# Kernel tuning notes

Hardware: AMD Instinct MI355X
Metric: run time of the kernel (lower is better)

The kernel has to match this reference:

```python
import jax, jax.numpy as jnp
import numpy as np
import math

B, N, D, K = 8, 2048, 1024, 128
PI = math.pi


def setup_inputs() -> dict:
    key = jax.random.key(0)
    ks = jax.random.split(key, 4)
    x = jax.random.normal(ks[0], (B, N, D), dtype=jnp.float32)
    W_proj = jax.random.normal(ks[1], (D, 6 * K), dtype=jnp.float32) * (D ** -0.5)
    # structured bias init as in OscillatorProjection._init_weights
    b = np.zeros(6 * K, np.float32)
    groups = [K // 4, K // 2, K - K // 4 - K // 2]
    centers = [0.3, 0.65, 0.97]
    off = 3 * K
    for n_k, c in zip(groups, centers):
        b[off:off + n_k] = math.log(c / (1.0 - c))
        off += n_k
    b[4 * K:5 * K] = math.log(0.65 / 0.35)
    b[5 * K:] = -2.0
    b_proj = jnp.asarray(b)
    omega_base = jnp.exp(jnp.linspace(math.log(2.0 * PI / N), math.log(PI * (1.0 - 1.0 / K)), K)).astype(jnp.float32)
    W_phase = jax.random.normal(ks[2], (D, K), dtype=jnp.float32) * 0.001
    b_phase = jnp.zeros((K,), jnp.float32)
    W_res = jax.random.normal(ks[3], (4 * K - 2, D), dtype=jnp.float32) * 0.002
    lambda_pcg = jnp.float32(0.5)
    res_scale = jnp.float32(0.05)
    return dict(x=x, W_proj=W_proj, b_proj=b_proj, omega_base=omega_base,
                W_phase=W_phase, b_phase=b_phase, W_res=W_res,
                lambda_pcg=lambda_pcg, res_scale=res_scale)


def _resonance_scan(alpha, drive):
    # linear recurrence r_t = alpha_t * r_{t-1} + d_t, r_0 = 0, along axis=1
    def combine(e1, e2):
        a1, b1 = e1
        a2, b2 = e2
        return (a2 * a1, a2 * b1 + b2)
    _, r = jax.lax.associative_scan(combine, (alpha, drive), axis=1)
    return r


def reference(x, W_proj, b_proj, omega_base, W_phase, b_phase, W_res, lambda_pcg, res_scale):
    _, n, _ = x.shape
    out = x @ W_proj + b_proj  # [B, n, 6K]
    A_r, Om_r, Ph_r, Ga_r, Go_r, Be_r = jnp.split(out, 6, axis=-1)
    A = jnp.minimum(jax.nn.softplus(A_r), 3.0)
    omega = jnp.clip(jax.nn.sigmoid(Om_r) * PI + omega_base, 1e-4, PI - 1e-4)
    phi = jnp.tanh(Ph_r) * PI
    alpha = jax.nn.sigmoid(Ga_r)
    g_out = jax.nn.sigmoid(Go_r)
    beta = jax.nn.sigmoid(Be_r)
    positions = jnp.log1p(jnp.arange(n, dtype=jnp.float32)).reshape(1, n, 1)
    angle = omega * positions + phi
    cos_a = jnp.cos(angle)
    sin_a = jnp.sin(angle)
    drive = (1.0 - alpha) * A
    # fused real/imag scan sharing alpha (mirrors the fused Triton path)
    r = _resonance_scan(jnp.concatenate([alpha, alpha], axis=-1),
                        jnp.concatenate([drive * cos_a, drive * sin_a], axis=-1))
    r_r, r_i = r[..., :K], r[..., K:]
    readout = r_r * cos_a + r_i * sin_a
    r_r = r_r - beta * readout * cos_a
    r_i = r_i - beta * readout * sin_a
    # state norm: rescale only when |r| > 1
    modulus = jnp.sqrt(r_r ** 2 + r_i ** 2 + 1e-8)
    scale = jnp.maximum(modulus, 1.0)
    r_r = r_r / scale
    r_i = r_i / scale
    # rotate into the oscillator frame
    rho_re = r_r * cos_a + r_i * sin_a
    rho_im = -r_r * sin_a + r_i * cos_a
    rho_norm = jnp.sqrt(rho_re ** 2 + rho_im ** 2 + 1e-6)
    pq = x @ W_phase + b_phase
    align = (rho_re * jnp.cos(pq) + rho_im * jnp.sin(pq)) / rho_norm
    gate = jax.nn.sigmoid(lambda_pcg * align)
    rho_re = gate * rho_re
    rho_im = gate * rho_im
    # SCPM: adjacent-oscillator complex cross products -> 4K-2 features
    cross_re = rho_re[..., :-1] * rho_re[..., 1:] + rho_im[..., :-1] * rho_im[..., 1:]
    cross_im = rho_im[..., :-1] * rho_re[..., 1:] - rho_re[..., :-1] * rho_im[..., 1:]
    feats = jnp.concatenate([g_out * rho_re, g_out * rho_im, cross_re, cross_im], axis=-1)
    return x + res_scale * (feats @ W_res)
```

## Files before the change

### kernel.cpp

```cpp
#include <hip/hip_runtime.h>
#include <math.h>

#define PI_F 3.14159265358979323846f
#define SEG 128
#define SLEN 16
typedef unsigned short u16;
typedef __attribute__((ext_vector_type(8))) short bf16x8;
typedef __attribute__((ext_vector_type(4))) float f32x4;

__device__ __forceinline__ float sigmoidf_(float x){ return __fdividef(1.0f, 1.0f+__expf(-x)); }
__device__ __forceinline__ float softplusf_(float x){
    return fmaxf(x, 0.f) + __logf(1.f + __expf(-fabsf(x)));
}
__device__ __forceinline__ float tanhpi_(float x){
    float t = __expf(-2.f*fabsf(x));
    float th = __fdividef(1.f - t, 1.f + t);
    return copysignf(th, x)*PI_F;
}
__device__ __forceinline__ void fsincos(float a, float* s, float* c){
    float r = a * 0.15915494309189535f;
    r = r - floorf(r);
#if __has_builtin(__builtin_amdgcn_sinf)
    *s = __builtin_amdgcn_sinf(r);
    *c = __builtin_amdgcn_cosf(r);
#else
    float t = r * 6.283185307179586f;
    *s = __sinf(t); *c = __cosf(t);
#endif
}
__device__ __forceinline__ u16 f2bf(float f){
    unsigned u = __float_as_uint(f);
    return (u16)((u + 0x7FFFu + ((u>>16)&1u)) >> 16);
}
__device__ __forceinline__ float b2f(u16 v){
    return __uint_as_float(((unsigned)v)<<16);
}
__device__ __forceinline__ void gl_lds16(const u16* g, u16* l){
    __builtin_amdgcn_global_load_lds((const __attribute__((address_space(1))) void*)g,
                                     (__attribute__((address_space(3))) void*)l, 16, 0, 0);
}

__global__ __launch_bounds__(256) void k_cvt_x(const float* __restrict__ x, u16* __restrict__ xb){
    size_t i = ((size_t)blockIdx.x*256 + threadIdx.x)*8;
    float4 v0 = *(const float4*)&x[i];
    float4 v1 = *(const float4*)&x[i+4];
    ushort4 a = make_ushort4(f2bf(v0.x),f2bf(v0.y),f2bf(v0.z),f2bf(v0.w));
    ushort4 b = make_ushort4(f2bf(v1.x),f2bf(v1.y),f2bf(v1.z),f2bf(v1.w));
    *(ushort4*)&xb[i]   = a;
    *(ushort4*)&xb[i+4] = b;
}

__global__ __launch_bounds__(256) void k_tcvt(const float* __restrict__ W, u16* __restrict__ Wt,
                                              int K, int Ns, int KD){
    __shared__ float s[32][33];
    const int tx = threadIdx.x & 31, ty = threadIdx.x >> 5;
    const int k0 = blockIdx.y*32, n0 = blockIdx.x*32;
    #pragma unroll
    for (int i=0;i<4;i++){
        int k = k0 + ty + i*8;
        s[ty+i*8][tx] = (k < K) ? W[(size_t)k*Ns + n0 + tx] : 0.f;
    }
    __syncthreads();
    #pragma unroll
    for (int i=0;i<4;i++){
        int n = n0 + ty + i*8;
        Wt[(size_t)n*KD + k0 + tx] = f2bf(s[tx][ty+i*8]);
    }
}

__global__ __launch_bounds__(256) void k_mm1(
    const u16* __restrict__ A,
    const u16* __restrict__ Bt,
    const float* __restrict__ bp, const float* __restrict__ bph,
    u16* __restrict__ C)
{
    const int bid = blockIdx.x;
    const int swz = (bid & 7)*112 + (bid >> 3);
    const int by = swz / 7, bx = swz - by*7;

    __shared__ u16 As[128*32];
    __shared__ u16 Bs[128*32];
    const int tid = threadIdx.x;
    const int w = tid>>6, lane = tid&63;
    const int wm = w>>1, wn = w&1;
    const int r0 = by*128, c0 = bx*128;

    const u16* ga[2]; const u16* gb[2]; u16 *la[2], *lb[2];
    #pragma unroll
    for (int i=0;i<2;i++){
        ga[i] = A  + (size_t)(r0 + w*32 + i*16 + (lane>>2))*1024 + (lane&3)*8;
        gb[i] = Bt + (size_t)(c0 + w*32 + i*16 + (lane>>2))*1024 + (lane&3)*8;
        la[i] = As + w*1024 + i*512;
        lb[i] = Bs + w*1024 + i*512;
    }
    const int lr = lane&15, lk = lane>>4;
    const int ao = (wm*64 + lr)*32 + lk*8;
    const int bo = (wn*64 + lr)*32 + lk*8;

    f32x4 acc[4][4] = {};
    for (int k0=0; k0<1024; k0+=32){
        gl_lds16(ga[0]+k0, la[0]); gl_lds16(ga[1]+k0, la[1]);
        gl_lds16(gb[0]+k0, lb[0]); gl_lds16(gb[1]+k0, lb[1]);
        __syncthreads();
        bf16x8 af[4], bfr[4];
        #pragma unroll
        for (int m=0;m<4;m++) af[m]  = *(const bf16x8*)&As[ao + m*512];
        #pragma unroll
        for (int n=0;n<4;n++) bfr[n] = *(const bf16x8*)&Bs[bo + n*512];
        #pragma unroll
        for (int m=0;m<4;m++)
            #pragma unroll
            for (int n=0;n<4;n++)
                acc[m][n] = __builtin_amdgcn_mfma_f32_16x16x32_bf16(af[m], bfr[n], acc[m][n], 0,0,0);
        __syncthreads();
    }
    #pragma unroll
    for (int n=0;n<4;n++){
        int col = c0 + wn*64 + n*16 + lr;
        float bl = (col < 768) ? bp[col] : bph[col-768];
        #pragma unroll
        for (int m=0;m<4;m++){
            int row = r0 + wm*64 + m*16 + lk*4;
            #pragma unroll
            for (int r=0;r<4;r++)
                C[(size_t)(row+r)*896 + col] = f2bf(acc[m][n][r] + bl);
        }
    }
}

__global__ __launch_bounds__(256) void k_mm2(
    const u16* __restrict__ A,
    const u16* __restrict__ Bt,
    const float* __restrict__ X,
    const float* __restrict__ rs_p,
    float* __restrict__ O)
{
    const int bid = blockIdx.x;
    const int swz = (bid & 7)*128 + (bid >> 3);
    const int by = swz >> 3, bx = swz & 7;

    __shared__ u16 As[128*32];
    __shared__ u16 Bs[128*32];
    const int tid = threadIdx.x;
    const int w = tid>>6, lane = tid&63;
    const int wm = w>>1, wn = w&1;
    const int r0 = by*128, c0 = bx*128;

    const u16* ga[2]; const u16* gb[2]; u16 *la[2], *lb[2];
    #pragma unroll
    for (int i=0;i<2;i++){
        ga[i] = A  + (size_t)(r0 + w*32 + i*16 + (lane>>2))*512 + (lane&3)*8;
        gb[i] = Bt + (size_t)(c0 + w*32 + i*16 + (lane>>2))*512 + (lane&3)*8;
        la[i] = As + w*1024 + i*512;
        lb[i] = Bs + w*1024 + i*512;
    }
    const int lr = lane&15, lk = lane>>4;
    const int ao = (wm*64 + lr)*32 + lk*8;
    const int bo = (wn*64 + lr)*32 + lk*8;

    f32x4 acc[4][4] = {};
    for (int k0=0; k0<512; k0+=32){
        gl_lds16(ga[0]+k0, la[0]); gl_lds16(ga[1]+k0, la[1]);
        gl_lds16(gb[0]+k0, lb[0]); gl_lds16(gb[1]+k0, lb[1]);
        __syncthreads();
        bf16x8 af[4], bfr[4];
        #pragma unroll
        for (int m=0;m<4;m++) af[m]  = *(const bf16x8*)&As[ao + m*512];
        #pragma unroll
        for (int n=0;n<4;n++) bfr[n] = *(const bf16x8*)&Bs[bo + n*512];
        #pragma unroll
        for (int m=0;m<4;m++)
            #pragma unroll
            for (int n=0;n<4;n++)
                acc[m][n] = __builtin_amdgcn_mfma_f32_16x16x32_bf16(af[m], bfr[n], acc[m][n], 0,0,0);
        __syncthreads();
    }
    const float rs = rs_p[0];
    #pragma unroll
    for (int n=0;n<4;n++){
        int col = c0 + wn*64 + n*16 + lr;
        #pragma unroll
        for (int m=0;m<4;m++){
            int row = r0 + wm*64 + m*16 + lk*4;
            #pragma unroll
            for (int r=0;r<4;r++){
                size_t idx = (size_t)(row+r)*1024 + col;
                O[idx] = X[idx] + rs*acc[m][n][r];
            }
        }
    }
}

__global__ __launch_bounds__(128) void k_s1(
    const u16* __restrict__ C1,
    const float* __restrict__ omega_base,
    float* __restrict__ Ag, float* __restrict__ Br, float* __restrict__ Bi)
{
    const int k = threadIdx.x;
    const int seg = blockIdx.x, b = blockIdx.y;
    const float ob = omega_base[k];
    const int n0 = seg*SLEN;
    float aag = 1.f, br = 0.f, bi = 0.f;
    #pragma unroll 4
    for (int s=0; s<SLEN; s++){
        const int n = n0 + s;
        const u16* row = C1 + (size_t)(b*2048+n)*896;
        float Ar = b2f(row[k]);
        float Om = b2f(row[128+k]);
        float Ph = b2f(row[256+k]);
        float Ga = b2f(row[384+k]);
        float alpha = sigmoidf_(Ga);
        float A = fminf(softplusf_(Ar), 3.0f);
        float omega = fminf(fmaxf(sigmoidf_(Om)*PI_F + ob, 1e-4f), PI_F-1e-4f);
        float phi = tanhpi_(Ph);
        float pos = __logf(1.f + (float)n);
        float sa, ca; fsincos(fmaf(omega, pos, phi), &sa, &ca);
        float drive = (1.f-alpha)*A;
        aag *= alpha;
        br = fmaf(alpha, br, drive*ca);
        bi = fmaf(alpha, bi, drive*sa);
    }
    const size_t o = (size_t)(b*SEG + seg)*128 + k;
    Ag[o] = aag; Br[o] = br; Bi[o] = bi;
}

__global__ __launch_bounds__(256) void k_s2(
    const float* __restrict__ Ag, const float* __restrict__ Br, const float* __restrict__ Bi,
    float* __restrict__ Pr, float* __restrict__ Pi)
{
    const int gid = blockIdx.x*256 + threadIdx.x;
    const int b = gid >> 7, k = gid & 127;
    float pr = 0.f, pi = 0.f;
    #pragma unroll 8
    for (int seg=0; seg<SEG; seg++){
        const size_t o = (size_t)(b*SEG + seg)*128 + k;
        float a = Ag[o], r = Br[o], i = Bi[o];
        Pr[o] = pr; Pi[o] = pi;
        pr = fmaf(a, pr, r);
        pi = fmaf(a, pi, i);
    }
}

__global__ __launch_bounds__(128) void k_s3(
    const u16* __restrict__ C1,
    const float* __restrict__ omega_base,
    const float* __restrict__ lam_p,
    const float* __restrict__ Pr, const float* __restrict__ Pi,
    u16* __restrict__ F)
{
    const int k = threadIdx.x;
    const int seg = blockIdx.x, b = blockIdx.y;
    const float ob = omega_base[k];
    const float lam = lam_p[0];
    __shared__ float sre[2][129], sim[2][129];

    const size_t po = (size_t)(b*SEG + seg)*128 + k;
    float rr = Pr[po], ri = Pi[po];
    const int n0 = seg*SLEN;

    #pragma unroll 2
    for (int s=0; s<SLEN; s++){
        const int n = n0 + s;
        const u16* row = C1 + (size_t)(b*2048+n)*896;
        float Ar = b2f(row[k]);
        float Om = b2f(row[128+k]);
        float Ph = b2f(row[256+k]);
        float Ga = b2f(row[384+k]);
        float Go = b2f(row[512+k]);
        float Be = b2f(row[640+k]);
        float pq = b2f(row[768+k]);
        float alpha = sigmoidf_(Ga);
        float A = fminf(softplusf_(Ar), 3.0f);
        float omega = fminf(fmaxf(sigmoidf_(Om)*PI_F + ob, 1e-4f), PI_F-1e-4f);
        float phi = tanhpi_(Ph);
        float pos = __logf(1.f + (float)n);
        float sa, ca; fsincos(fmaf(omega, pos, phi), &sa, &ca);
        float drive = (1.f-alpha)*A;
        rr = fmaf(alpha, rr, drive*ca);
        ri = fmaf(alpha, ri, drive*sa);
        float readout = rr*ca + ri*sa;
        float beta = sigmoidf_(Be);
        float r2r = rr - beta*readout*ca;
        float r2i = ri - beta*readout*sa;
        float m2 = r2r*r2r + r2i*r2i + 1e-8f;
        float inv = fminf(rsqrtf(m2), 1.0f);
        r2r *= inv; r2i *= inv;
        float rho_re =  r2r*ca + r2i*sa;
        float rho_im = -r2r*sa + r2i*ca;
        float rho2 = rho_re*rho_re + rho_im*rho_im + 1e-6f;
        float spq, cpq; fsincos(pq, &spq, &cpq);
        float align = (rho_re*cpq + rho_im*spq)*rsqrtf(rho2);
        float gate = sigmoidf_(lam*align);
        rho_re *= gate; rho_im *= gate;
        float go = sigmoidf_(Go);

        const int buf = s & 1;
        sre[buf][k] = rho_re; sim[buf][k] = rho_im;
        __syncthreads();

        u16* frow = F + (size_t)(b*2048+n)*512;
        frow[k]       = f2bf(go*rho_re);
        frow[128 + k] = f2bf(go*rho_im);
        if (k < 127){
            float nre = sre[buf][k+1], nim = sim[buf][k+1];
            frow[256 + k] = f2bf(rho_re*nre + rho_im*nim);
            frow[383 + k] = f2bf(rho_im*nre - rho_re*nim);
        } else {
            frow[510] = 0; frow[511] = 0;
        }
    }
}

extern "C" void kernel_launch(void* const* d_in, const int* in_sizes, int n_in,
                              void* d_out, int out_size, void* d_ws, size_t ws_size,
                              hipStream_t stream)
{
    const float* x   = (const float*)d_in[0];
    const float* Wp  = (const float*)d_in[1];
    const float* bp  = (const float*)d_in[2];
    const float* ob  = (const float*)d_in[3];
    const float* Wph = (const float*)d_in[4];
    const float* bph = (const float*)d_in[5];
    const float* Wr  = (const float*)d_in[6];
    const float* lam = (const float*)d_in[7];
    const float* rs  = (const float*)d_in[8];
    float* out = (float*)d_out;

    char* ws = (char*)d_ws;
    u16*   C1  = (u16*)  (ws + 0);
    u16*   Xb  = (u16*)  (ws + 58720256);
    float* Ag  = (float*)(ws + 58720256);
    float* Brr = (float*)(ws + 58720256 +  524288);
    float* Bii = (float*)(ws + 58720256 + 1048576);
    float* Pr  = (float*)(ws + 58720256 + 1572864);
    float* Pi  = (float*)(ws + 58720256 + 2097152);
    u16*   F   = (u16*)  (ws + 58720256 + 2621440);
    u16*   Wt  = (u16*)  (ws + 92274688);
    u16*   Wrt = (u16*)  (ws + 94109696);

    dim3 blk(256);
    hipLaunchKernelGGL(k_cvt_x, dim3(8192),   blk, 0, stream, x, Xb);
    hipLaunchKernelGGL(k_tcvt,  dim3(24,32),  blk, 0, stream, Wp,  Wt,            1024, 768,  1024);
    hipLaunchKernelGGL(k_tcvt,  dim3(4,32),   blk, 0, stream, Wph, Wt + 768*1024, 1024, 128,  1024);
    hipLaunchKernelGGL(k_tcvt,  dim3(32,16),  blk, 0, stream, Wr,  Wrt,           510,  1024, 512);
    hipLaunchKernelGGL(k_mm1,   dim3(896),    blk, 0, stream, Xb, Wt, bp, bph, C1);
    hipLaunchKernelGGL(k_s1,    dim3(SEG,8),  dim3(128), 0, stream, C1, ob, Ag, Brr, Bii);
    hipLaunchKernelGGL(k_s2,    dim3(4),      blk, 0, stream, Ag, Brr, Bii, Pr, Pi);
    hipLaunchKernelGGL(k_s3,    dim3(SEG,8),  dim3(128), 0, stream, C1, ob, lam, Pr, Pi, F);
    hipLaunchKernelGGL(k_mm2,   dim3(1024),   blk, 0, stream, F, Wrt, x, rs, out);
}
```

Measured before the change: 152.7 us.

## Fuse three scan kernels into one cooperative kernel with grid syncs and LDS staging

Replaces the three-pass segmented scan (local reduce, carry propagation, apply) with a single cooperative kernel. Each block stages its 16×896 bf16 slice of C1 in shared memory once, so the second pass no longer rereads global memory. Two grid-wide syncs separate the phases, and only 8 blocks run the serial carry scan. The workspace buffers are moved so the bf16 copy of x stays alive, and the final GEMM epilogue now reads that bf16 x instead of fp32 x. That lowers residual precision and adds grid-sync overhead plus a co-residency requirement for 1024 blocks.

After: 318.4 us. 109% more time.

```diff
diff --git a/kernel.cpp b/kernel.cpp
--- a/kernel.cpp
+++ b/kernel.cpp
@@ -1,11 +1,15 @@
 #include <hip/hip_runtime.h>
+#include <hip/hip_cooperative_groups.h>
 #include <math.h>
+
+namespace cg = cooperative_groups;
 
 #define PI_F 3.14159265358979323846f
 #define SEG 128
 #define SLEN 16
 typedef unsigned short u16;
 typedef __attribute__((ext_vector_type(8))) short bf16x8;
+typedef __attribute__((ext_vector_type(8))) unsigned short u16x8;
 typedef __attribute__((ext_vector_type(4))) float f32x4;
 
 __device__ __forceinline__ float sigmoidf_(float x){ return __fdividef(1.0f, 1.0f+__expf(-x)); }
@@ -131,7 +135,7 @@
 __global__ __launch_bounds__(256) void k_mm2(
     const u16* __restrict__ A,
     const u16* __restrict__ Bt,
-    const float* __restrict__ X,
+    const u16* __restrict__ Xb,
     const float* __restrict__ rs_p,
     float* __restrict__ O)
 {
@@ -185,90 +189,92 @@
             #pragma unroll
             for (int r=0;r<4;r++){
                 size_t idx = (size_t)(row+r)*1024 + col;
-                O[idx] = X[idx] + rs*acc[m][n][r];
+                O[idx] = b2f(Xb[idx]) + rs*acc[m][n][r];
             }
         }
     }
 }
 
-__global__ __launch_bounds__(128) void k_s1(
-    const u16* __restrict__ C1,
-    const float* __restrict__ omega_base,
-    float* __restrict__ Ag, float* __restrict__ Br, float* __restrict__ Bi)
-{
-    const int k = threadIdx.x;
-    const int seg = blockIdx.x, b = blockIdx.y;
-    const float ob = omega_base[k];
-    const int n0 = seg*SLEN;
-    float aag = 1.f, br = 0.f, bi = 0.f;
-    #pragma unroll 4
-    for (int s=0; s<SLEN; s++){
-        const int n = n0 + s;
-        const u16* row = C1 + (size_t)(b*2048+n)*896;
-        float Ar = b2f(row[k]);
-        float Om = b2f(row[128+k]);
-        float Ph = b2f(row[256+k]);
-        float Ga = b2f(row[384+k]);
-        float alpha = sigmoidf_(Ga);
-        float A = fminf(softplusf_(Ar), 3.0f);
-        float omega = fminf(fmaxf(sigmoidf_(Om)*PI_F + ob, 1e-4f), PI_F-1e-4f);
-        float phi = tanhpi_(Ph);
-        float pos = __logf(1.f + (float)n);
-        float sa, ca; fsincos(fmaf(omega, pos, phi), &sa, &ca);
-        float drive = (1.f-alpha)*A;
-        aag *= alpha;
-        br = fmaf(alpha, br, drive*ca);
-        bi = fmaf(alpha, bi, drive*sa);
-    }
-    const size_t o = (size_t)(b*SEG + seg)*128 + k;
-    Ag[o] = aag; Br[o] = br; Bi[o] = bi;
-}
-
-__global__ __launch_bounds__(256) void k_s2(
-    const float* __restrict__ Ag, const float* __restrict__ Br, const float* __restrict__ Bi,
-    float* __restrict__ Pr, float* __restrict__ Pi)
-{
-    const int gid = blockIdx.x*256 + threadIdx.x;
-    const int b = gid >> 7, k = gid & 127;
-    float pr = 0.f, pi = 0.f;
-    #pragma unroll 8
-    for (int seg=0; seg<SEG; seg++){
-        const size_t o = (size_t)(b*SEG + seg)*128 + k;
-        float a = Ag[o], r = Br[o], i = Bi[o];
-        Pr[o] = pr; Pi[o] = pi;
-        pr = fmaf(a, pr, r);
-        pi = fmaf(a, pi, i);
-    }
-}
-
-__global__ __launch_bounds__(128) void k_s3(
+__global__ __launch_bounds__(128) void k_scan_fused(
     const u16* __restrict__ C1,
     const float* __restrict__ omega_base,
     const float* __restrict__ lam_p,
-    const float* __restrict__ Pr, const float* __restrict__ Pi,
+    float* __restrict__ Ag, float* __restrict__ Br, float* __restrict__ Bi,
+    float* __restrict__ Pr, float* __restrict__ Pi,
     u16* __restrict__ F)
 {
     const int k = threadIdx.x;
     const int seg = blockIdx.x, b = blockIdx.y;
     const float ob = omega_base[k];
     const float lam = lam_p[0];
+
+    __shared__ u16 sC[16][896];
     __shared__ float sre[2][129], sim[2][129];
 
-    const size_t po = (size_t)(b*SEG + seg)*128 + k;
-    float rr = Pr[po], ri = Pi[po];
+    {
+        const u16* src = C1 + (size_t)(b*2048 + seg*SLEN)*896;
+        #pragma unroll
+        for (int c=0; c<14; ++c){
+            int chunk = c*128 + k;
+            int r = chunk / 112;
+            int off = (chunk - r*112)*8;
+            *(u16x8*)&sC[r][off] = *(const u16x8*)&src[(size_t)r*896 + off];
+        }
+    }
+    __syncthreads();
+
     const int n0 = seg*SLEN;
-
+    float aag = 1.f, br = 0.f, bi = 0.f;
+    #pragma unroll 4
+    for (int s=0; s<SLEN; s++){
+        float Ar = b2f(sC[s][k]);
+        float Om = b2f(sC[s][128+k]);
+        float Ph = b2f(sC[s][256+k]);
+        float Ga = b2f(sC[s][384+k]);
+        float alpha = sigmoidf_(Ga);
+        float A = fminf(softplusf_(Ar), 3.0f);
+        float omega = fminf(fmaxf(sigmoidf_(Om)*PI_F + ob, 1e-4f), PI_F-1e-4f);
+        float phi = tanhpi_(Ph);
+        float pos = __logf(1.f + (float)(n0+s));
+        float sa, ca; fsincos(fmaf(omega, pos, phi), &sa, &ca);
+        float drive = (1.f-alpha)*A;
+        aag *= alpha;
+        br = fmaf(alpha, br, drive*ca);
+        bi = fmaf(alpha, bi, drive*sa);
+    }
+    const size_t o = (size_t)(b*SEG + seg)*128 + k;
+    Ag[o] = aag; Br[o] = br; Bi[o] = bi;
+
+    cg::this_grid().sync();
+
+    const int fb = b*gridDim.x + seg;
+    if (fb < 8){
+        const int gid = fb*128 + k;
+        const int bb = gid >> 7, kk = gid & 127;
+        float pr = 0.f, pi = 0.f;
+        #pragma unroll 8
+        for (int sg=0; sg<SEG; sg++){
+            const size_t oo = (size_t)(bb*SEG + sg)*128 + kk;
+            float a = Ag[oo], r = Br[oo], i = Bi[oo];
+            Pr[oo] = pr; Pi[oo] = pi;
+            pr = fmaf(a, pr, r);
+            pi = fmaf(a, pi, i);
+        }
+    }
+
+    cg::this_grid().sync();
+
+    float rr = Pr[o], ri = Pi[o];
     #pragma unroll 2
     for (int s=0; s<SLEN; s++){
         const int n = n0 + s;
-        const u16* row = C1 + (size_t)(b*2048+n)*896;
-        float Ar = b2f(row[k]);
-        float Om = b2f(row[128+k]);
-        float Ph = b2f(row[256+k]);
-        float Ga = b2f(row[384+k]);
-        float Go = b2f(row[512+k]);
-        float Be = b2f(row[640+k]);
-        float pq = b2f(row[768+k]);
+        float Ar = b2f(sC[s][k]);
+        float Om = b2f(sC[s][128+k]);
+        float Ph = b2f(sC[s][256+k]);
+        float Ga = b2f(sC[s][384+k]);
+        float Go = b2f(sC[s][512+k]);
+        float Be = b2f(sC[s][640+k]);
+        float pq = b2f(sC[s][768+k]);
         float alpha = sigmoidf_(Ga);
         float A = fminf(softplusf_(Ar), 3.0f);
         float omega = fminf(fmaxf(sigmoidf_(Om)*PI_F + ob, 1e-4f), PI_F-1e-4f);
@@ -328,13 +334,13 @@
 
     char* ws = (char*)d_ws;
     u16*   C1  = (u16*)  (ws + 0);
+    float* Ag  = (float*)(ws + 29360128);
+    float* Brr = (float*)(ws + 29884416);
+    float* Bii = (float*)(ws + 30408704);
+    float* Pr  = (float*)(ws + 30932992);
+    float* Pi  = (float*)(ws + 31457280);
+    u16*   F   = (u16*)  (ws + 31981568);
     u16*   Xb  = (u16*)  (ws + 58720256);
-    float* Ag  = (float*)(ws + 58720256);
-    float* Brr = (float*)(ws + 58720256 +  524288);
-    float* Bii = (float*)(ws + 58720256 + 1048576);
-    float* Pr  = (float*)(ws + 58720256 + 1572864);
-    float* Pi  = (float*)(ws + 58720256 + 2097152);
-    u16*   F   = (u16*)  (ws + 58720256 + 2621440);
     u16*   Wt  = (u16*)  (ws + 92274688);
     u16*   Wrt = (u16*)  (ws + 94109696);
 
@@ -344,8 +350,13 @@
     hipLaunchKernelGGL(k_tcvt,  dim3(4,32),   blk, 0, stream, Wph, Wt + 768*1024, 1024, 128,  1024);
     hipLaunchKernelGGL(k_tcvt,  dim3(32,16),  blk, 0, stream, Wr,  Wrt,           510,  1024, 512);
     hipLaunchKernelGGL(k_mm1,   dim3(896),    blk, 0, stream, Xb, Wt, bp, bph, C1);
-    hipLaunchKernelGGL(k_s1,    dim3(SEG,8),  dim3(128), 0, stream, C1, ob, Ag, Brr, Bii);
-    hipLaunchKernelGGL(k_s2,    dim3(4),      blk, 0, stream, Ag, Brr, Bii, Pr, Pi);
-    hipLaunchKernelGGL(k_s3,    dim3(SEG,8),  dim3(128), 0, stream, C1, ob, lam, Pr, Pi, F);
-    hipLaunchKernelGGL(k_mm2,   dim3(1024),   blk, 0, stream, F, Wrt, x, rs, out);
-}
+
+    const u16* C1c = C1;
+    void* args[] = { (void*)&C1c, (void*)&ob, (void*)&lam,
+                     (void*)&Ag, (void*)&Brr, (void*)&Bii,
+                     (void*)&Pr, (void*)&Pi, (void*)&F };
+    hipLaunchCooperativeKernel((const void*)k_scan_fused, dim3(SEG,8), dim3(128),
+                               args, 0, stream);
+
+    hipLaunchKernelGGL(k_mm2,   dim3(1024),   blk, 0, stream, F, Wrt, Xb, rs, out);
+}
```
